# Optimization experiments

Hardware: AMD Instinct MI355X
Metric: run time of the kernel (lower is better)

## Reference

```python
import jax, jax.numpy as jnp
import numpy as np


def conv2d(x, w, b):
    # NCHW input, OIHW kernel, SAME padding, stride 1
    y = jax.lax.conv_general_dilated(x, w, (1, 1), 'SAME',
                                     dimension_numbers=('NCHW', 'OIHW', 'NCHW'))
    return y + b[None, :, None, None]


def maxpool2(x):
    return jax.lax.reduce_window(x, -jnp.inf, jax.lax.max,
                                 (1, 1, 2, 2), (1, 1, 2, 2), 'VALID')


def gelu(x):
    return jax.nn.gelu(x, approximate=False)  # torch default exact GELU


def up2(x):
    # nearest-neighbor upsample x2 (torch Upsample mode='nearest')
    return jnp.repeat(jnp.repeat(x, 2, axis=2), 2, axis=3)


DIM = 32
CODEBOOK_SIZE = 512
COMMIT_W = 1.0


def setup_inputs() -> dict:
    key = jax.random.key(0)
    ks = jax.random.split(key, 10)
    s = 0.1
    return {
        'x': jax.random.normal(ks[0], (32, 1, 256, 256), jnp.float32),
        'e1_w': jax.random.normal(ks[1], (16, 1, 3, 3), jnp.float32) * s,
        'e1_b': jnp.zeros((16,), jnp.float32),
        'e2_w': jax.random.normal(ks[2], (32, 16, 3, 3), jnp.float32) * s,
        'e2_b': jnp.zeros((32,), jnp.float32),
        'codebook': jax.random.normal(ks[3], (CODEBOOK_SIZE, DIM), jnp.float32),
        'd1_w': jax.random.normal(ks[4], (16, 32, 3, 3), jnp.float32) * s,
        'd1_b': jnp.zeros((16,), jnp.float32),
        'd2_w': jax.random.normal(ks[5], (1, 16, 3, 3), jnp.float32) * s,
        'd2_b': jnp.zeros((1,), jnp.float32),
    }


def reference(x, e1_w, e1_b, e2_w, e2_b, codebook, d1_w, d1_b, d2_w, d2_b):
    # ---- encoder ----
    h = conv2d(x, e1_w, e1_b)
    h = maxpool2(h)
    h = gelu(h)
    h = conv2d(h, e2_w, e2_b)
    h = maxpool2(h)                      # [B, 32, H/4, W/4]

    # ---- vector quantize (accept_image_fmap=True) ----
    B, C, H, W = h.shape
    flat = h.transpose(0, 2, 3, 1).reshape(-1, C)          # [N, C] tokens
    # squared euclidean distances to codebook
    d = ((flat * flat).sum(-1, keepdims=True)
         - 2.0 * flat @ codebook.T
         + (codebook * codebook).sum(-1))                   # [N, K]
    idx = jnp.argmin(d, axis=-1)                            # [N] int
    q = codebook[idx]                                       # gather [N, C]
    commit_loss = COMMIT_W * jnp.mean((jax.lax.stop_gradient(q) - flat) ** 2)
    # straight-through estimator
    q = flat + jax.lax.stop_gradient(q - flat)
    hq = q.reshape(B, H, W, C).transpose(0, 3, 1, 2)        # back to NCHW
    indices = idx.reshape(B, H, W)

    # ---- decoder ----
    y = up2(hq)
    y = conv2d(y, d1_w, d1_b)
    y = gelu(y)
    y = up2(y)
    y = conv2d(y, d2_w, d2_b)
    return jnp.clip(y, -1.0, 1.0), indices, commit_loss
```

## Files before the change

### kernel.cpp

```cpp
#include <hip/hip_runtime.h>
#include <math.h>

#define GELU(v) (0.5f * (v) * (1.0f + erff((v)*0.70710678118654752440f)))

typedef __attribute__((ext_vector_type(8))) short short8;
typedef __attribute__((ext_vector_type(4))) float f32x4;
typedef __attribute__((ext_vector_type(16))) float f32x16;
#define MFMA16 __builtin_amdgcn_mfma_f32_16x16x32_bf16
#define MFMA32 __builtin_amdgcn_mfma_f32_32x32x16_bf16

#define SPLIT3(V, U1, U2, U3)                                                  \
  unsigned U1 = __float_as_uint(V) & 0xFFFF0000u;                              \
  float _r1 = (V)-__uint_as_float(U1);                                         \
  unsigned U2 = __float_as_uint(_r1) & 0xFFFF0000u;                            \
  float _r2 = _r1 - __uint_as_float(U2);                                       \
  unsigned U3 = __float_as_uint(_r2) & 0xFFFF0000u;

#define H1PL 8388608

__global__ __launch_bounds__(256) void k_fold(const float* __restrict__ e2w,
                                              const float* __restrict__ d1w,
                                              const float* __restrict__ d2w,
                                              const float* __restrict__ cb,
                                              float* __restrict__ fwd2,
                                              unsigned short* __restrict__ cbs,
                                              float* __restrict__ csqg,
                                              unsigned short* __restrict__ wfrag,
                                              unsigned short* __restrict__ wfd1,
                                              float* __restrict__ lossout) {
  int i = blockIdx.x * 256 + threadIdx.x;
  if (i == 0) lossout[0] = 0.f;
  if (i < 256) {
    int j = i;
    int pt = j & 15, ic = j >> 4;
    int a = pt >> 3, b2 = (pt >> 2) & 1, dy = (pt >> 1) & 1, dx = pt & 1;
    const float* wsrc = d2w + ic * 9;
    float s = 0.f;
    for (int ky = 0; ky < 3; ++ky) {
      int rm = (a == 0) ? (ky == 0 ? 0 : 1) : (ky == 2 ? 1 : 0);
      if (rm != dy) continue;
      for (int kx = 0; kx < 3; ++kx) {
        int cm = (b2 == 0) ? (kx == 0 ? 0 : 1) : (kx == 2 ? 1 : 0);
        if (cm == dx) s += wsrc[ky * 3 + kx];
      }
    }
    fwd2[j] = s;
  } else if (i < 16640) {
    int j = i - 256;
    float v = cb[j];
    SPLIT3(v, u1, u2, u3)
    cbs[j] = (unsigned short)(u1 >> 16);
    cbs[16384 + j] = (unsigned short)(u2 >> 16);
    cbs[32768 + j] = (unsigned short)(u3 >> 16);
  } else if (i < 17152) {
    int c = i - 16640;
    const float* row = cb + (size_t)c * 32;
    float s = 0.f;
#pragma unroll
    for (int d = 0; d < 32; ++d) s = fmaf(row[d], row[d], s);
    csqg[c] = s;
  } else if (i < 30976) {
    int j = i - 17152;
    int p = j / 4608, rem = j - p * 4608;
    int t = rem >> 9, l2 = (rem >> 3) & 63, jj = rem & 7;
    float v = e2w[((l2 & 31) * 16 + ((l2 >> 5) * 8 + jj)) * 9 + t];
    SPLIT3(v, u1, u2, u3)
    unsigned short r = (p == 0)   ? (unsigned short)(u1 >> 16)
                       : (p == 1) ? (unsigned short)(u2 >> 16)
                                  : (unsigned short)(u3 >> 16);
    wfrag[j] = r;
  } else if (i < 86272) {
    int j = i - 30976;
    int slot = j >> 9, l2 = (j >> 3) & 63, jj = j & 7;
    int cx = slot / 36, rem = slot % 36;
    int r3 = rem / 12, rem2 = rem % 12;
    int kh = rem2 / 6, rem3 = rem2 % 6;
    int pp = rem3 / 3, part = rem3 % 3;
    int c = l2 & 31, hi = l2 >> 5;
    int oc = c & 15, b2 = c >> 4;
    int ic = kh * 16 + hi * 8 + jj;
    int dy = r3 - pp, dx = cx - b2;
    float s = 0.f;
    if ((unsigned)dy < 2u && (unsigned)dx < 2u) {
      const float* wsrc = d1w + (oc * 32 + ic) * 9;
      for (int ky = 0; ky < 3; ++ky) {
        int rm = (pp == 0) ? (ky == 0 ? 0 : 1) : (ky == 2 ? 1 : 0);
        if (rm != dy) continue;
        for (int kx = 0; kx < 3; ++kx) {
          int cm = (b2 == 0) ? (kx == 0 ? 0 : 1) : (kx == 2 ? 1 : 0);
          if (cm == dx) s += wsrc[ky * 3 + kx];
        }
      }
    }
    SPLIT3(s, u1, u2, u3)
    unsigned short r = (part == 0)   ? (unsigned short)(u1 >> 16)
                       : (part == 1) ? (unsigned short)(u2 >> 16)
                                     : (unsigned short)(u3 >> 16);
    wfd1[j] = r;
  }
}

__global__ __launch_bounds__(256) void k_enc1(const float* __restrict__ x,
                                              const float* __restrict__ w,
                                              const float* __restrict__ bias,
                                              unsigned short* __restrict__ h1s) {
  int n = blockIdx.x;
  int ysl = n & 7, m = n >> 3;
  int b = m & 31, k = m >> 5;
  int yy = ysl * 16 + k * 2 + (threadIdx.x >> 7);
  int xx = threadIdx.x & 127;
  const float* xp = x + (size_t)b * 65536;
  int r0 = 2 * yy - 1, c0 = 2 * xx - 1;
  float in[4][4];
#pragma unroll
  for (int i = 0; i < 4; ++i) {
    int r = r0 + i;
    bool rv = (unsigned)r < 256u;
#pragma unroll
    for (int j = 0; j < 4; ++j) {
      int c = c0 + j;
      in[i][j] = (rv && (unsigned)c < 256u) ? xp[r * 256 + c] : 0.0f;
    }
  }
  short8 p1[2], p2[2], p3[2];
#pragma unroll
  for (int oc = 0; oc < 16; ++oc) {
    const float* wp = w + oc * 9;
    float s00 = 0.f, s01 = 0.f, s10 = 0.f, s11 = 0.f;
#pragma unroll
    for (int ky = 0; ky < 3; ++ky)
#pragma unroll
      for (int kx = 0; kx < 3; ++kx) {
        float wv = wp[ky * 3 + kx];
        s00 = fmaf(in[ky][kx], wv, s00);
        s01 = fmaf(in[ky][kx + 1], wv, s01);
        s10 = fmaf(in[ky + 1][kx], wv, s10);
        s11 = fmaf(in[ky + 1][kx + 1], wv, s11);
      }
    float mm = fmaxf(fmaxf(s00, s01), fmaxf(s10, s11)) + bias[oc];
    float g = GELU(mm);
    SPLIT3(g, u1, u2, u3)
    p1[oc >> 3][oc & 7] = (short)(u1 >> 16);
    p2[oc >> 3][oc & 7] = (short)(u2 >> 16);
    p3[oc >> 3][oc & 7] = (short)(u3 >> 16);
  }
  unsigned short* op = h1s + (size_t)b * 262144 + ((size_t)yy * 128 + xx) * 16;
  *(short8*)(op) = p1[0];
  *(short8*)(op + 8) = p1[1];
  *(short8*)(op + H1PL) = p2[0];
  *(short8*)(op + H1PL + 8) = p2[1];
  *(short8*)(op + 2 * H1PL) = p3[0];
  *(short8*)(op + 2 * H1PL + 8) = p3[1];
}

__global__ __launch_bounds__(256) void k_enc2(const unsigned short* __restrict__ h1s,
                                              const unsigned short* __restrict__ wfrag,
                                              const float* __restrict__ bias,
                                              float* __restrict__ h2) {
  __shared__ __align__(16) unsigned short sA[3 * 2 * 10 * 34 * 8];
  const int PP = 2 * 10 * 34 * 8;
  int tid = threadIdx.x;
  int n = blockIdx.x;
  int xcd = n & 7, m = n >> 3;
  int ty = xcd * 2 + (m & 1);
  int q0 = m >> 1;
  int b = q0 >> 2, xt = q0 & 3;
  int X0 = xt * 32, Y0 = ty * 8;
  const unsigned short* ip = h1s + (size_t)b * 262144;
  for (int g = tid; g < 680; g += 256) {
    int pos = g >> 1, ich = g & 1;
    int yy = pos / 34, xx = pos - yy * 34;
    int y = Y0 - 1 + yy, xg = X0 - 1 + xx;
    short8 v1 = {0, 0, 0, 0, 0, 0, 0, 0};
    short8 v2 = {0, 0, 0, 0, 0, 0, 0, 0};
    short8 v3 = {0, 0, 0, 0, 0, 0, 0, 0};
    if ((unsigned)y < 128u && (unsigned)xg < 128u) {
      const unsigned short* sp = ip + ((size_t)y * 128 + xg) * 16 + ich * 8;
      v1 = *(const short8*)(sp);
      v2 = *(const short8*)(sp + H1PL);
      v3 = *(const short8*)(sp + 2 * H1PL);
    }
    int si = ((ich * 10 + yy) * 34 + xx) * 8;
    *(short8*)(sA + si) = v1;
    *(short8*)(sA + PP + si) = v2;
    *(short8*)(sA + 2 * PP + si) = v3;
  }
  __syncthreads();

  int l = tid & 63, w = tid >> 6;
  int xl = l & 31, ich = l >> 5;
  f32x16 acc0[2], acc1[2];
#pragma unroll
  for (int s = 0; s < 2; ++s)
#pragma unroll
    for (int r = 0; r < 16; ++r) { acc0[s][r] = 0.f; acc1[s][r] = 0.f; }

#pragma unroll
  for (int t = 0; t < 9; ++t) {
    int dy = t / 3, dx = t % 3;
    int s = t & 1;
    const unsigned short* wb = wfrag + t * 512 + l * 8;
    short8 bf1 = *(const short8*)(wb);
    short8 bf2 = *(const short8*)(wb + 4608);
    short8 bf3 = *(const short8*)(wb + 9216);
    int g0 = ((ich * 10) + (2 * w + dy)) * 34 + xl + dx;
    const unsigned short* a0p = sA + g0 * 8;
    short8 a01 = *(const short8*)(a0p);
    short8 a02 = *(const short8*)(a0p + PP);
    short8 a03 = *(const short8*)(a0p + 2 * PP);
    const unsigned short* a1p = a0p + 34 * 8;
    short8 a11 = *(const short8*)(a1p);
    short8 a12 = *(const short8*)(a1p + PP);
    short8 a13 = *(const short8*)(a1p + 2 * PP);
    acc0[s] = MFMA32(a01, bf1, acc0[s], 0, 0, 0);
    acc0[s] = MFMA32(a01, bf2, acc0[s], 0, 0, 0);
    acc0[s] = MFMA32(a02, bf1, acc0[s], 0, 0, 0);
    acc0[s] = MFMA32(a02, bf2, acc0[s], 0, 0, 0);
    acc0[s] = MFMA32(a01, bf3, acc0[s], 0, 0, 0);
    acc0[s] = MFMA32(a03, bf1, acc0[s], 0, 0, 0);
    acc1[s] = MFMA32(a11, bf1, acc1[s], 0, 0, 0);
    acc1[s] = MFMA32(a11, bf2, acc1[s], 0, 0, 0);
    acc1[s] = MFMA32(a12, bf1, acc1[s], 0, 0, 0);
    acc1[s] = MFMA32(a12, bf2, acc1[s], 0, 0, 0);
    acc1[s] = MFMA32(a11, bf3, acc1[s], 0, 0, 0);
    acc1[s] = MFMA32(a13, bf1, acc1[s], 0, 0, 0);
  }

  float bv = bias[l & 31];
  int ypool = (Y0 >> 1) + w;
  float* op = h2 + (size_t)b * 131072 + (size_t)(l & 31) * 4096 + ypool * 64 + (X0 >> 1);
#pragma unroll
  for (int k = 0; k < 8; ++k) {
    float e0 = (acc0[0][2 * k] + acc0[1][2 * k]);
    float o0 = (acc0[0][2 * k + 1] + acc0[1][2 * k + 1]);
    float e1 = (acc1[0][2 * k] + acc1[1][2 * k]);
    float o1 = (acc1[0][2 * k + 1] + acc1[1][2 * k + 1]);
    float mm = fmaxf(fmaxf(e0, o0), fmaxf(e1, o1)) + bv;
    int row = ((2 * k) & 3) + 8 * ((2 * k) >> 2) + 4 * ich;
    op[row >> 1] = mm;
  }
}

__global__ __launch_bounds__(256) void k_vq(const float* __restrict__ h2,
                                            const unsigned short* __restrict__ cbs,
                                            const float* __restrict__ csqg,
                                            float* __restrict__ idxout,
                                            float* __restrict__ lossout) {
  __shared__ __align__(16) unsigned short sA[3 * 256 * 40];
  __shared__ float sFsq[256];
  __shared__ float sBd[256];
  __shared__ int sBi[256];
  __shared__ float sred[4];
  int tid = threadIdx.x;
  int blk = blockIdx.x;
  int t0 = blk * 256;
  size_t abase = (size_t)(t0 >> 12) * 131072 + (t0 & 4095);

  {
    const float* src = h2 + abase + tid;
    float fsq = 0.f;
#pragma unroll
    for (int g = 0; g < 4; ++g) {
      short8 p1, p2, p3;
#pragma unroll
      for (int e = 0; e < 8; ++e) {
        float v = src[(g * 8 + e) * 4096];
        fsq = fmaf(v, v, fsq);
        SPLIT3(v, u1, u2, u3)
        p1[e] = (short)(u1 >> 16);
        p2[e] = (short)(u2 >> 16);
        p3[e] = (short)(u3 >> 16);
      }
      *(short8*)(sA + (0 * 256 + tid) * 40 + g * 8) = p1;
      *(short8*)(sA + (1 * 256 + tid) * 40 + g * 8) = p2;
      *(short8*)(sA + (2 * 256 + tid) * 40 + g * 8) = p3;
    }
    sFsq[tid] = fsq;
  }
  __syncthreads();

  int l = tid & 63, w = tid >> 6;
  int cl = l & 15, k0 = (l >> 4) * 8;
  short8 af[3][4];
#pragma unroll
  for (int p = 0; p < 3; ++p)
#pragma unroll
    for (int tq = 0; tq < 4; ++tq) {
      int tok = w * 64 + tq * 16 + cl;
      af[p][tq] = *(const short8*)(sA + (p * 256 + tok) * 40 + k0);
    }

  float bd[4][4];
  int bi[4][4];
#pragma unroll
  for (int a = 0; a < 4; ++a)
#pragma unroll
    for (int b = 0; b < 4; ++b) { bd[a][b] = 3.4e38f; bi[a][b] = 0; }

#define LOADB(S, CT)                                                           \
  {                                                                            \
    int col = (CT)*16 + cl;                                                    \
    b1##S = *(const short8*)(cbs + (0 * 512 + col) * 32 + k0);                 \
    b2##S = *(const short8*)(cbs + (1 * 512 + col) * 32 + k0);                 \
    b3##S = *(const short8*)(cbs + (2 * 512 + col) * 32 + k0);                 \
    cq##S = csqg[col];                                                         \
  }
#define COMPUTE(S, CT)                                                         \
  {                                                                            \
    _Pragma("unroll") for (int tq = 0; tq < 4; ++tq) {                         \
      f32x4 acc = {0.f, 0.f, 0.f, 0.f};                                        \
      acc = MFMA16(af[0][tq], b1##S, acc, 0, 0, 0);                            \
      acc = MFMA16(af[0][tq], b2##S, acc, 0, 0, 0);                            \
      acc = MFMA16(af[1][tq], b1##S, acc, 0, 0, 0);                            \
      acc = MFMA16(af[1][tq], b2##S, acc, 0, 0, 0);                            \
      acc = MFMA16(af[0][tq], b3##S, acc, 0, 0, 0);                            \
      acc = MFMA16(af[2][tq], b1##S, acc, 0, 0, 0);                            \
      _Pragma("unroll") for (int i = 0; i < 4; ++i) {                          \
        float d = fmaf(-2.f, acc[i], cq##S);                                   \
        if (d < bd[tq][i]) { bd[tq][i] = d; bi[tq][i] = (CT)*16 + cl; }        \
      }                                                                        \
    }                                                                          \
  }

  short8 b1A, b2A, b3A, b1B, b2B, b3B;
  float cqA, cqB;
  LOADB(A, 0)
  LOADB(B, 1)
#pragma unroll 1
  for (int ct = 0; ct < 32; ct += 2) {
    COMPUTE(A, ct)
    LOADB(A, (ct + 2) & 31)
    COMPUTE(B, ct + 1)
    LOADB(B, (ct + 3) & 31)
  }
#undef LOADB
#undef COMPUTE

#pragma unroll
  for (int tq = 0; tq < 4; ++tq)
#pragma unroll
    for (int i = 0; i < 4; ++i)
#pragma unroll
      for (int m = 1; m < 16; m <<= 1) {
        float od = __shfl_xor(bd[tq][i], m, 64);
        int ob = __shfl_xor(bi[tq][i], m, 64);
        if (od < bd[tq][i] || (od == bd[tq][i] && ob < bi[tq][i])) {
          bd[tq][i] = od;
          bi[tq][i] = ob;
        }
      }
  if (cl == 0) {
#pragma unroll
    for (int tq = 0; tq < 4; ++tq)
#pragma unroll
      for (int i = 0; i < 4; ++i) {
        int tokl = w * 64 + tq * 16 + (l >> 4) * 4 + i;
        sBi[tokl] = bi[tq][i];
        sBd[tokl] = bd[tq][i];
      }
  }
  __syncthreads();

  idxout[t0 + tid] = (float)sBi[tid];
  float loss = sBd[tid] + sFsq[tid];
#pragma unroll
  for (int off = 32; off > 0; off >>= 1) loss += __shfl_down(loss, off, 64);
  if (l == 0) sred[w] = loss;
  __syncthreads();
  if (tid == 0)
    atomicAdd(lossout, ((sred[0] + sred[1]) + (sred[2] + sred[3])) * (1.0f / 4194304.0f));
}

__global__ __launch_bounds__(256) void k_dec1(const float* __restrict__ idxf,
                                              const unsigned short* __restrict__ cbs,
                                              const unsigned short* __restrict__ wfd1,
                                              const float* __restrict__ bias,
                                              float* __restrict__ o) {
  __shared__ int sIdx[204];
  int tid = threadIdx.x;
  int b = blockIdx.y;
  int qx0 = (blockIdx.x & 1) * 32, qy0 = (blockIdx.x >> 1) * 4;
  const float* ib = idxf + (size_t)b * 4096;
  if (tid < 204) {
    int yy = tid / 34, xx = tid % 34;
    int y = qy0 - 1 + yy, x = qx0 - 1 + xx;
    sIdx[tid] = ((unsigned)y < 64u && (unsigned)x < 64u) ? (int)ib[y * 64 + x] : -1;
  }
  __syncthreads();

  int l = tid & 63, w = tid >> 6;
  int xl = l & 31, hi = l >> 5;
  f32x16 acc[2];
#pragma unroll
  for (int p2 = 0; p2 < 2; ++p2)
#pragma unroll
    for (int r = 0; r < 16; ++r) acc[p2][r] = 0.f;

#pragma unroll
  for (int cx = 0; cx < 3; ++cx) {
#pragma unroll
    for (int kh = 0; kh < 2; ++kh) {
      short8 Bf[4][3];
#pragma unroll
      for (int q = 0; q < 4; ++q) {
        int r3 = (q == 0) ? 0 : (q == 3) ? 2 : 1;
        int pq = (q >= 2) ? 1 : 0;
#pragma unroll
        for (int pt = 0; pt < 3; ++pt) {
          int slot = cx * 36 + r3 * 12 + kh * 6 + pq * 3 + pt;
          Bf[q][pt] = *(const short8*)(wfd1 + (size_t)slot * 512 + l * 8);
        }
      }
#pragma unroll
      for (int ry = 0; ry < 3; ++ry) {
        int idx = sIdx[(w + ry) * 34 + xl + cx];
        short8 a1 = {0, 0, 0, 0, 0, 0, 0, 0};
        short8 a2 = {0, 0, 0, 0, 0, 0, 0, 0};
        short8 a3 = {0, 0, 0, 0, 0, 0, 0, 0};
        if (idx >= 0) {
          const unsigned short* ap = cbs + (size_t)idx * 32 + kh * 16 + hi * 8;
          a1 = *(const short8*)(ap);
          a2 = *(const short8*)(ap + 16384);
          a3 = *(const short8*)(ap + 32768);
        }
#pragma unroll
        for (int p2 = 0; p2 < 2; ++p2) {
          if ((ry == 0 && p2 == 1) || (ry == 2 && p2 == 0)) continue;
          int q = ry + p2;
          f32x16 t = acc[p2];
          t = MFMA32(a1, Bf[q][0], t, 0, 0, 0);
          t = MFMA32(a1, Bf[q][1], t, 0, 0, 0);
          t = MFMA32(a2, Bf[q][0], t, 0, 0, 0);
          t = MFMA32(a2, Bf[q][1], t, 0, 0, 0);
          t = MFMA32(a1, Bf[q][2], t, 0, 0, 0);
          t = MFMA32(a3, Bf[q][0], t, 0, 0, 0);
          acc[p2] = t;
        }
      }
    }
  }

  float bv = bias[l & 15];
  int b2 = (l >> 4) & 1;
  int oc = l & 15;
  int qy = qy0 + w;
  float* ob = o + (size_t)b * 262144;
#pragma unroll
  for (int p2 = 0; p2 < 2; ++p2) {
    int Y = 2 * qy + p2;
#pragma unroll
    for (int reg = 0; reg < 16; ++reg) {
      int rowval = (reg & 3) + 8 * (reg >> 2) + 4 * hi;
      int X = qx0 * 2 + 2 * rowval + b2;
      ob[((size_t)Y * 128 + X) * 16 + oc] = GELU(acc[p2][reg] + bv);
    }
  }
}

__device__ __forceinline__ void d2_loadi3(float (&dst)[3][3], const float* t) {
#pragma unroll
  for (int dy = 0; dy < 3; ++dy)
#pragma unroll
    for (int dx = 0; dx < 3; ++dx) dst[dy][dx] = t[(dy * 18 + dx) * 17];
}
__global__ __launch_bounds__(256) void k_dec2(const float* __restrict__ d1,
                                              const float* __restrict__ fwd2,
                                              const float* __restrict__ bias,
                                              float* __restrict__ out) {
  __shared__ float st[18 * 18 * 17];
  int tid = threadIdx.x;
  int b = blockIdx.y;
  int R0 = (blockIdx.x >> 3) * 16, C0 = (blockIdx.x & 7) * 16;
  const float* ip = d1 + (size_t)b * 262144;
  for (int i = tid; i < 1296; i += 256) {
    int pos = i >> 2, q = i & 3;
    int rr = pos / 18, cc = pos % 18;
    int r = R0 - 1 + rr, c = C0 - 1 + cc;
    float4 v = {0.f, 0.f, 0.f, 0.f};
    if ((unsigned)r < 128u && (unsigned)c < 128u)
      v = *(const float4*)(ip + ((size_t)r * 128 + c) * 16 + q * 4);
    float* dp = st + (rr * 18 + cc) * 17 + q * 4;
    dp[0] = v.x; dp[1] = v.y; dp[2] = v.z; dp[3] = v.w;
  }
  __syncthreads();
  int lane = tid & 63, wid = tid >> 6;
  int qy = wid >> 1, qx = wid & 1;
  int ty = qy * 8 + (lane >> 3), tx = qx * 8 + (lane & 7);
  float acc[4] = {0.f, 0.f, 0.f, 0.f};
  const float* tb = st + (ty * 18 + tx) * 17;
  float i3A[3][3], i3B[3][3];
  d2_loadi3(i3A, tb);
#pragma unroll 1
  for (int ic = 0; ic < 16; ic += 2) {
    d2_loadi3(i3B, tb + (ic + 1));
    {
      const float* wp = fwd2 + ic * 16;
#pragma unroll
      for (int p = 0; p < 4; ++p) {
        int a = p >> 1, b2 = p & 1;
#pragma unroll
        for (int tp = 0; tp < 4; ++tp) {
          int dy = tp >> 1, dx = tp & 1;
          acc[p] = fmaf(i3A[a + dy][b2 + dx], wp[p * 4 + tp], acc[p]);
        }
      }
    }
    d2_loadi3(i3A, tb + ((ic + 2) & 15));
    {
      const float* wp = fwd2 + (ic + 1) * 16;
#pragma unroll
      for (int p = 0; p < 4; ++p) {
        int a = p >> 1, b2 = p & 1;
#pragma unroll
        for (int tp = 0; tp < 4; ++tp) {
          int dy = tp >> 1, dx = tp & 1;
          acc[p] = fmaf(i3B[a + dy][b2 + dx], wp[p * 4 + tp], acc[p]);
        }
      }
    }
  }
  float bv = bias[0];
  int Y = 2 * (R0 + ty), X = 2 * (C0 + tx);
  float* op = out + (size_t)b * 65536 + Y * 256 + X;
  float2 r0v, r1v;
  r0v.x = fminf(1.0f, fmaxf(-1.0f, acc[0] + bv));
  r0v.y = fminf(1.0f, fmaxf(-1.0f, acc[1] + bv));
  r1v.x = fminf(1.0f, fmaxf(-1.0f, acc[2] + bv));
  r1v.y = fminf(1.0f, fmaxf(-1.0f, acc[3] + bv));
  *(float2*)op = r0v;
  *(float2*)(op + 256) = r1v;
}

extern "C" void kernel_launch(void* const* d_in, const int* in_sizes, int n_in,
                              void* d_out, int out_size, void* d_ws, size_t ws_size,
                              hipStream_t stream) {
  const float* x   = (const float*)d_in[0];
  const float* e1w = (const float*)d_in[1];
  const float* e1b = (const float*)d_in[2];
  const float* e2w = (const float*)d_in[3];
  const float* e2b = (const float*)d_in[4];
  const float* cb  = (const float*)d_in[5];
  const float* d1w = (const float*)d_in[6];
  const float* d1b = (const float*)d_in[7];
  const float* d2w = (const float*)d_in[8];
  const float* d2b = (const float*)d_in[9];

  float* out = (float*)d_out;
  float* y       = out;
  float* idxout  = out + 2097152;
  float* lossout = out + 2097152 + 131072;

  float* ws = (float*)d_ws;
  unsigned short* h1s = (unsigned short*)ws;
  float* h2      = ws + 12582912;
  float* fwd2    = ws + 16777216;
  float* d1o     = ws;

  unsigned short* cbs = (unsigned short*)out;
  float* csqg = out + 24576;
  unsigned short* wfrag = (unsigned short*)(out + 25088);
  unsigned short* wfd1 = (unsigned short*)(out + 32000);

  k_fold<<<dim3(337), 256, 0, stream>>>(e2w, d1w, d2w, cb, fwd2, cbs, csqg, wfrag, wfd1, lossout);
  k_enc1<<<dim3(2048), 256, 0, stream>>>(x, e1w, e1b, h1s);
  k_enc2<<<dim3(2048), 256, 0, stream>>>(h1s, wfrag, e2b, h2);
  k_vq<<<dim3(512), 256, 0, stream>>>(h2, cbs, csqg, idxout, lossout);
  k_dec1<<<dim3(32, 32), 256, 0, stream>>>(idxout, cbs, wfd1, d1b, d1o);
  k_dec2<<<dim3(64, 32), 256, 0, stream>>>(d1o, fwd2, d2b, y);
}
```

Baseline: 211.9 us.

## Halve VQ block token tile and load A fragments directly from global

```diff
diff --git a/kernel.cpp b/kernel.cpp
--- a/kernel.cpp
+++ b/kernel.cpp
@@ -241,59 +241,54 @@
   }
 }
 
-__global__ __launch_bounds__(256) void k_vq(const float* __restrict__ h2,
-                                            const unsigned short* __restrict__ cbs,
-                                            const float* __restrict__ csqg,
-                                            float* __restrict__ idxout,
-                                            float* __restrict__ lossout) {
-  __shared__ __align__(16) unsigned short sA[3 * 256 * 40];
-  __shared__ float sFsq[256];
-  __shared__ float sBd[256];
-  __shared__ int sBi[256];
-  __shared__ float sred[4];
+__global__ __launch_bounds__(256, 4) void k_vq(const float* __restrict__ h2,
+                                               const unsigned short* __restrict__ cbs,
+                                               const float* __restrict__ csqg,
+                                               float* __restrict__ idxout,
+                                               float* __restrict__ lossout) {
+  __shared__ float sFsq[128];
+  __shared__ float sBd[128];
+  __shared__ int sBi[128];
+  __shared__ float sred[2];
   int tid = threadIdx.x;
   int blk = blockIdx.x;
-  int t0 = blk * 256;
+  int t0 = blk * 128;
   size_t abase = (size_t)(t0 >> 12) * 131072 + (t0 & 4095);
-
-  {
-    const float* src = h2 + abase + tid;
-    float fsq = 0.f;
-#pragma unroll
-    for (int g = 0; g < 4; ++g) {
-      short8 p1, p2, p3;
-#pragma unroll
-      for (int e = 0; e < 8; ++e) {
-        float v = src[(g * 8 + e) * 4096];
-        fsq = fmaf(v, v, fsq);
-        SPLIT3(v, u1, u2, u3)
-        p1[e] = (short)(u1 >> 16);
-        p2[e] = (short)(u2 >> 16);
-        p3[e] = (short)(u3 >> 16);
-      }
-      *(short8*)(sA + (0 * 256 + tid) * 40 + g * 8) = p1;
-      *(short8*)(sA + (1 * 256 + tid) * 40 + g * 8) = p2;
-      *(short8*)(sA + (2 * 256 + tid) * 40 + g * 8) = p3;
-    }
-    sFsq[tid] = fsq;
-  }
-  __syncthreads();
 
   int l = tid & 63, w = tid >> 6;
   int cl = l & 15, k0 = (l >> 4) * 8;
-  short8 af[3][4];
-#pragma unroll
-  for (int p = 0; p < 3; ++p)
-#pragma unroll
-    for (int tq = 0; tq < 4; ++tq) {
-      int tok = w * 64 + tq * 16 + cl;
-      af[p][tq] = *(const short8*)(sA + (p * 256 + tok) * 40 + k0);
-    }
-
-  float bd[4][4];
-  int bi[4][4];
-#pragma unroll
-  for (int a = 0; a < 4; ++a)
+
+  short8 af1[2], af2[2], af3[2];
+  float fsq[2];
+#pragma unroll
+  for (int tq = 0; tq < 2; ++tq) {
+    const float* src = h2 + abase + w * 32 + tq * 16 + cl;
+    float fs = 0.f;
+#pragma unroll
+    for (int e = 0; e < 8; ++e) {
+      float v = src[(size_t)(k0 + e) * 4096];
+      fs = fmaf(v, v, fs);
+      SPLIT3(v, u1, u2, u3)
+      af1[tq][e] = (short)(u1 >> 16);
+      af2[tq][e] = (short)(u2 >> 16);
+      af3[tq][e] = (short)(u3 >> 16);
+    }
+    fsq[tq] = fs;
+  }
+#pragma unroll
+  for (int tq = 0; tq < 2; ++tq) {
+    fsq[tq] += __shfl_xor(fsq[tq], 16, 64);
+    fsq[tq] += __shfl_xor(fsq[tq], 32, 64);
+  }
+  if (l < 16) {
+    sFsq[w * 32 + l] = fsq[0];
+    sFsq[w * 32 + 16 + l] = fsq[1];
+  }
+
+  float bd[2][4];
+  int bi[2][4];
+#pragma unroll
+  for (int a = 0; a < 2; ++a)
 #pragma unroll
     for (int b = 0; b < 4; ++b) { bd[a][b] = 3.4e38f; bi[a][b] = 0; }
 
@@ -307,14 +302,14 @@
   }
 #define COMPUTE(S, CT)                                                         \
   {                                                                            \
-    _Pragma("unroll") for (int tq = 0; tq < 4; ++tq) {                         \
+    _Pragma("unroll") for (int tq = 0; tq < 2; ++tq) {                         \
       f32x4 acc = {0.f, 0.f, 0.f, 0.f};                                        \
-      acc = MFMA16(af[0][tq], b1##S, acc, 0, 0, 0);                            \
-      acc = MFMA16(af[0][tq], b2##S, acc, 0, 0, 0);                            \
-      acc = MFMA16(af[1][tq], b1##S, acc, 0, 0, 0);                            \
-      acc = MFMA16(af[1][tq], b2##S, acc, 0, 0, 0);                            \
-      acc = MFMA16(af[0][tq], b3##S, acc, 0, 0, 0);                            \
-      acc = MFMA16(af[2][tq], b1##S, acc, 0, 0, 0);                            \
+      acc = MFMA16(af1[tq], b1##S, acc, 0, 0, 0);                              \
+      acc = MFMA16(af1[tq], b2##S, acc, 0, 0, 0);                              \
+      acc = MFMA16(af2[tq], b1##S, acc, 0, 0, 0);                              \
+      acc = MFMA16(af2[tq], b2##S, acc, 0, 0, 0);                              \
+      acc = MFMA16(af1[tq], b3##S, acc, 0, 0, 0);                              \
+      acc = MFMA16(af3[tq], b1##S, acc, 0, 0, 0);                              \
       _Pragma("unroll") for (int i = 0; i < 4; ++i) {                          \
         float d = fmaf(-2.f, acc[i], cq##S);                                   \
         if (d < bd[tq][i]) { bd[tq][i] = d; bi[tq][i] = (CT)*16 + cl; }        \
@@ -337,7 +332,7 @@
 #undef COMPUTE
 
 #pragma unroll
-  for (int tq = 0; tq < 4; ++tq)
+  for (int tq = 0; tq < 2; ++tq)
 #pragma unroll
     for (int i = 0; i < 4; ++i)
 #pragma unroll
@@ -351,24 +346,25 @@
       }
   if (cl == 0) {
 #pragma unroll
-    for (int tq = 0; tq < 4; ++tq)
+    for (int tq = 0; tq < 2; ++tq)
 #pragma unroll
       for (int i = 0; i < 4; ++i) {
-        int tokl = w * 64 + tq * 16 + (l >> 4) * 4 + i;
+        int tokl = w * 32 + tq * 16 + (l >> 4) * 4 + i;
         sBi[tokl] = bi[tq][i];
         sBd[tokl] = bd[tq][i];
       }
   }
   __syncthreads();
 
-  idxout[t0 + tid] = (float)sBi[tid];
-  float loss = sBd[tid] + sFsq[tid];
-#pragma unroll
-  for (int off = 32; off > 0; off >>= 1) loss += __shfl_down(loss, off, 64);
-  if (l == 0) sred[w] = loss;
+  if (tid < 128) {
+    idxout[t0 + tid] = (float)sBi[tid];
+    float loss = sBd[tid] + sFsq[tid];
+#pragma unroll
+    for (int off = 32; off > 0; off >>= 1) loss += __shfl_down(loss, off, 64);
+    if ((tid & 63) == 0) sred[tid >> 6] = loss;
+  }
   __syncthreads();
-  if (tid == 0)
-    atomicAdd(lossout, ((sred[0] + sred[1]) + (sred[2] + sred[3])) * (1.0f / 4194304.0f));
+  if (tid == 0) atomicAdd(lossout, (sred[0] + sred[1]) * (1.0f / 4194304.0f));
 }
 
 __global__ __launch_bounds__(256) void k_dec1(const float* __restrict__ idxf,
@@ -564,7 +560,7 @@
   k_fold<<<dim3(337), 256, 0, stream>>>(e2w, d1w, d2w, cb, fwd2, cbs, csqg, wfrag, wfd1, lossout);
   k_enc1<<<dim3(2048), 256, 0, stream>>>(x, e1w, e1b, h1s);
   k_enc2<<<dim3(2048), 256, 0, stream>>>(h1s, wfrag, e2b, h2);
-  k_vq<<<dim3(512), 256, 0, stream>>>(h2, cbs, csqg, idxout, lossout);
+  k_vq<<<dim3(1024), 256, 0, stream>>>(h2, cbs, csqg, idxout, lossout);
   k_dec1<<<dim3(32, 32), 256, 0, stream>>>(idxout, cbs, wfd1, d1b, d1o);
   k_dec2<<<dim3(64, 32), 256, 0, stream>>>(d1o, fwd2, d2b, y);
 }
```

Result: slower. 219.0 us (+3.3%).
